# Kernel tuning notes

Hardware: AMD Instinct MI355X
Metric: run time of the kernel (lower is better)

The kernel has to match this reference:

```python
import jax, jax.numpy as jnp
import numpy as np

N_NODES = 50000
N_EDGES = 1600000
IN_DIM = 128
HID = 128
OUT_DIM = 64
N_REL = 8


def _rgcn(x, src, dst, et, W, W0, num_nodes):
    # W: [R, in, out], per-relation transform; identical math to the torch
    # loop over unique relations (scatter-adds commute).
    xW = jnp.einsum('ni,rio->rno', x, W)          # [R, N, out]
    msgs = xW[et, src]                             # [E, out] gather per edge
    out = x @ W0 + jax.ops.segment_sum(msgs, dst, num_segments=num_nodes)
    deg = jax.ops.segment_sum(jnp.ones_like(dst, dtype=x.dtype), dst,
                              num_segments=num_nodes)
    deg = jnp.maximum(deg, 1.0)
    return out / deg[:, None]


def _group(x, src, dst, num_nodes, alpha, Wp, bp):
    agg = jax.ops.segment_sum(x[src], dst, num_segments=num_nodes)
    deg = jax.ops.segment_sum(jnp.ones_like(dst, dtype=x.dtype), dst,
                              num_segments=num_nodes)
    deg = jnp.maximum(deg, 1.0)
    agg = agg / deg[:, None]
    return x + alpha * (agg @ Wp + bp)


def setup_inputs() -> dict:
    key = jax.random.key(0)
    ks = jax.random.split(key, 16)
    x = jax.random.normal(ks[0], (N_NODES, IN_DIM), dtype=jnp.float32)
    edge_index = jax.random.randint(ks[1], (2, N_EDGES), 0, N_NODES)
    edge_type = jax.random.randint(ks[2], (N_EDGES,), 0, N_REL)
    s = 0.02
    return {
        'x': x,
        'edge_index': edge_index,
        'edge_type': edge_type,
        'W1': jax.random.normal(ks[3], (N_REL, IN_DIM, HID)) * s,
        'W01': jax.random.normal(ks[4], (IN_DIM, HID)) * s,
        'alpha1': jnp.float32(0.5),
        'proj1_w': jax.random.normal(ks[5], (HID, HID)) * s,
        'proj1_b': jnp.zeros((HID,), jnp.float32),
        'W2': jax.random.normal(ks[6], (N_REL, HID, HID)) * s,
        'W02': jax.random.normal(ks[7], (HID, HID)) * s,
        'alpha2': jnp.float32(0.5),
        'proj2_w': jax.random.normal(ks[8], (HID, HID)) * s,
        'proj2_b': jnp.zeros((HID,), jnp.float32),
        'out_w': jax.random.normal(ks[9], (HID, OUT_DIM)) * s,
        'out_b': jnp.zeros((OUT_DIM,), jnp.float32),
    }


def reference(x, edge_index, edge_type, W1, W01, alpha1, proj1_w, proj1_b,
              W2, W02, alpha2, proj2_w, proj2_b, out_w, out_b):
    n = x.shape[0]
    src, dst = edge_index[0], edge_index[1]
    h = _rgcn(x, src, dst, edge_type, W1, W01, n)
    h = jax.nn.relu(h)
    h = _group(h, src, dst, n, alpha1, proj1_w, proj1_b)
    h = _rgcn(h, src, dst, edge_type, W2, W02, n)
    h = jax.nn.relu(h)
    h = _group(h, src, dst, n, alpha2, proj2_w, proj2_b)
    return h @ out_w + out_b
```

## Files before the change

### kernel.cpp

```cpp
#include <hip/hip_runtime.h>
#include <hip/hip_bf16.h>

#define NN 50000
#define NE 1600000
#define NR 8
#define D 128
#define DOUT 64
#define NCB ((NN + 63) / 64)
#define NBLK 256
#define CH ((NE + NBLK - 1) / NBLK)
#define GRIDM ((NN + 63) / 64)

typedef __attribute__((ext_vector_type(8))) __bf16 bf16x8;
typedef __attribute__((ext_vector_type(4))) float f32x4;

__device__ __forceinline__ float bflo(unsigned u) { return __uint_as_float(u << 16); }
__device__ __forceinline__ float bfhi(unsigned u) { return __uint_as_float(u & 0xffff0000u); }
__device__ __forceinline__ unsigned f2bf_rne(float x) {
    unsigned u = __float_as_uint(x);
    return (u + 0x7fffu + ((u >> 16) & 1u)) >> 16;
}
__device__ __forceinline__ unsigned pack2(float a, float b) {
    return f2bf_rne(a) | (f2bf_rne(b) << 16);
}

__device__ __forceinline__ void gl2lds16(const void* g, void* l) {
    __builtin_amdgcn_global_load_lds(
        (const __attribute__((address_space(1))) unsigned int*)g,
        (__attribute__((address_space(3))) unsigned int*)l, 16, 0, 0);
}

__global__ __launch_bounds__(1024)
void k_cnt(const int* __restrict__ ei, int* __restrict__ cntmat) {
    __shared__ int h[NCB];
    const int blk = blockIdx.x, tid = threadIdx.x;
    for (int i = tid; i < NCB; i += 1024) h[i] = 0;
    __syncthreads();
    const int e0 = blk * CH, e1 = min(e0 + CH, NE);
    for (int e = e0 + tid; e < e1; e += 1024)
        atomicAdd(&h[ei[NE + e] >> 6], 1);
    __syncthreads();
    for (int i = tid; i < NCB; i += 1024) cntmat[i * NBLK + blk] = h[i];
}

__global__ __launch_bounds__(64)
void k_colscan(int* __restrict__ cntmat, int* __restrict__ colsum) {
    const int b = blockIdx.x, lane = threadIdx.x;
    int4 v = *reinterpret_cast<int4*>(cntmat + b * NBLK + lane * 4);
    int s = v.x + v.y + v.z + v.w;
    int e = s;
    #pragma unroll
    for (int o = 1; o < 64; o <<= 1) {
        int y = __shfl_up(e, o);
        if (lane >= o) e += y;
    }
    int excl = e - s;
    int4 w;
    w.x = excl; w.y = excl + v.x; w.z = excl + v.x + v.y; w.w = excl + v.x + v.y + v.z;
    *reinterpret_cast<int4*>(cntmat + b * NBLK + lane * 4) = w;
    if (lane == 63) colsum[b] = e;
}

__global__ __launch_bounds__(1024)
void k_bscan(const int* __restrict__ colsum, int* __restrict__ bstart,
             int* __restrict__ off) {
    __shared__ int s[1024];
    int t = threadIdx.x;
    int v = (t < NCB) ? colsum[t] : 0;
    s[t] = v;
    __syncthreads();
    for (int o = 1; o < 1024; o <<= 1) {
        int x = (t >= o) ? s[t - o] : 0;
        __syncthreads();
        s[t] += x;
        __syncthreads();
    }
    if (t < NCB) bstart[t] = s[t] - v;
    if (t == 0) { bstart[NCB] = NE; off[NN] = NE; }
}

__global__ __launch_bounds__(1024)
void k_pscatter(const int* __restrict__ ei, const int* __restrict__ et,
                const int* __restrict__ cntmat, const int* __restrict__ bstart,
                int* __restrict__ bck) {
    __shared__ int cur[NCB];
    const int blk = blockIdx.x, tid = threadIdx.x;
    for (int i = tid; i < NCB; i += 1024)
        cur[i] = bstart[i] + cntmat[i * NBLK + blk];
    __syncthreads();
    const int e0 = blk * CH, e1 = min(e0 + CH, NE);
    for (int e = e0 + tid; e < e1; e += 1024) {
        int dst = ei[NE + e];
        int pk = ((dst & 63) << 19) | (et[e] << 16) | ei[e];
        int p = atomicAdd(&cur[dst >> 6], 1);
        bck[p] = pk;
    }
}

__global__ __launch_bounds__(256)
void k_build(const int* __restrict__ bck, const int* __restrict__ cbase,
             int* __restrict__ off, float* __restrict__ invdeg,
             int* __restrict__ esrcF) {
    __shared__ int cnt[64];
    __shared__ int cur[64];
    __shared__ int sb[2];
    const int b = blockIdx.x;
    const int tid = threadIdx.x;
    if (tid < 64) cnt[tid] = 0;
    if (tid == 0) { sb[0] = cbase[b]; sb[1] = cbase[b + 1]; }
    __syncthreads();
    const int s0 = sb[0], s1 = sb[1];
    for (int i = s0 + tid; i < s1; i += 256)
        atomicAdd(&cnt[(bck[i] >> 19) & 63], 1);
    __syncthreads();
    if (tid < 64) {
        int c = cnt[tid];
        int x = c;
        #pragma unroll
        for (int o = 1; o < 64; o <<= 1) {
            int y = __shfl_up(x, o);
            if (tid >= o) x += y;
        }
        int excl = x - c;
        int gd = b * 64 + tid;
        if (gd < NN) {
            off[gd] = s0 + excl;
            invdeg[gd] = 1.0f / (float)max(c, 1);
        }
        cur[tid] = s0 + excl;
    }
    __syncthreads();
    for (int i = s0 + tid; i < s1; i += 256) {
        int pk = bck[i];
        int p = atomicAdd(&cur[(pk >> 19) & 63], 1);
        esrcF[p] = pk & 0x7FFFF;
    }
}


__global__ void k_prep_x(const float* __restrict__ X, unsigned* __restrict__ Xt) {
    int i = blockIdx.x * blockDim.x + threadIdx.x;
    if (i < NN * 64) {
        float2 f = reinterpret_cast<const float2*>(X)[i];
        Xt[i] = pack2(f.x, f.y);
    }
}

__global__ void k_prep_wcat(const float* __restrict__ W0, const float* __restrict__ Wr,
                            unsigned short* __restrict__ dst) {
    int i = blockIdx.x * blockDim.x + threadIdx.x;
    if (i < 128 * 1152) {
        int n = i / 1152, k = i % 1152;
        float v = (k < 128) ? W0[k * 128 + n] : Wr[(k - 128) * 128 + n];
        int kc = k >> 7, kl = k & 127;
        int e = kl ^ ((n & 7) << 3);
        dst[((size_t)kc * 128 + n) * 128 + e] = (unsigned short)f2bf_rne(v);
    }
}

__global__ void k_prep_wt(const float* __restrict__ src, unsigned short* __restrict__ dst,
                          int N) {
    int i = blockIdx.x * blockDim.x + threadIdx.x;
    if (i < N * 128) {
        int n = i >> 7, k = i & 127;
        int e = k ^ ((n & 7) << 3);
        dst[n * 128 + e] = (unsigned short)f2bf_rne(src[k * N + n]);
    }
}


#define LOAD8                                                            \
    int p0 = __builtin_amdgcn_readfirstlane(esrcF[j]);                   \
    int p1 = __builtin_amdgcn_readfirstlane(esrcF[j + 1]);               \
    int p2 = __builtin_amdgcn_readfirstlane(esrcF[j + 2]);               \
    int p3 = __builtin_amdgcn_readfirstlane(esrcF[j + 3]);               \
    int p4 = __builtin_amdgcn_readfirstlane(esrcF[j + 4]);               \
    int p5 = __builtin_amdgcn_readfirstlane(esrcF[j + 5]);               \
    int p6 = __builtin_amdgcn_readfirstlane(esrcF[j + 6]);               \
    int p7 = __builtin_amdgcn_readfirstlane(esrcF[j + 7]);               \
    unsigned u0 = Xt[(unsigned)(p0 & 0xffff) * 64 + lane];               \
    unsigned u1 = Xt[(unsigned)(p1 & 0xffff) * 64 + lane];               \
    unsigned u2 = Xt[(unsigned)(p2 & 0xffff) * 64 + lane];               \
    unsigned u3 = Xt[(unsigned)(p3 & 0xffff) * 64 + lane];               \
    unsigned u4 = Xt[(unsigned)(p4 & 0xffff) * 64 + lane];               \
    unsigned u5 = Xt[(unsigned)(p5 & 0xffff) * 64 + lane];               \
    unsigned u6 = Xt[(unsigned)(p6 & 0xffff) * 64 + lane];               \
    unsigned u7 = Xt[(unsigned)(p7 & 0xffff) * 64 + lane];

__global__ __launch_bounds__(256)
void k_aggw(const unsigned* __restrict__ Xt, unsigned* __restrict__ AW,
            const int* __restrict__ off, const int* __restrict__ esrcF) {
    const int wid = threadIdx.x >> 6, lane = threadIdx.x & 63;
    const int v = blockIdx.x * 4 + wid;
    if (v >= NN) return;
    const int s = off[v], e = off[v + 1];
    float l0 = 0, l1 = 0, l2 = 0, l3 = 0, l4 = 0, l5 = 0, l6 = 0, l7 = 0;
    float h0 = 0, h1 = 0, h2 = 0, h3 = 0, h4 = 0, h5 = 0, h6 = 0, h7 = 0;
#define ACCW(P, U)                                                       \
    do {                                                                 \
        float _lo = bflo(U), _hi = bfhi(U);                              \
        switch ((P) >> 16) {                                             \
            case 0: l0 += _lo; h0 += _hi; break;                         \
            case 1: l1 += _lo; h1 += _hi; break;                         \
            case 2: l2 += _lo; h2 += _hi; break;                         \
            case 3: l3 += _lo; h3 += _hi; break;                         \
            case 4: l4 += _lo; h4 += _hi; break;                         \
            case 5: l5 += _lo; h5 += _hi; break;                         \
            case 6: l6 += _lo; h6 += _hi; break;                         \
            default: l7 += _lo; h7 += _hi; break;                        \
        }                                                                \
    } while (0)
    for (int j = s; j < e; j += 8) {
        LOAD8
        ACCW(p0, u0);
        if (j + 1 < e) ACCW(p1, u1);
        if (j + 2 < e) ACCW(p2, u2);
        if (j + 3 < e) ACCW(p3, u3);
        if (j + 4 < e) ACCW(p4, u4);
        if (j + 5 < e) ACCW(p5, u5);
        if (j + 6 < e) ACCW(p6, u6);
        if (j + 7 < e) ACCW(p7, u7);
    }
#undef ACCW
    unsigned* o = AW + (size_t)v * 512 + lane;
    o[0]   = pack2(l0, h0);
    o[64]  = pack2(l1, h1);
    o[128] = pack2(l2, h2);
    o[192] = pack2(l3, h3);
    o[256] = pack2(l4, h4);
    o[320] = pack2(l5, h5);
    o[384] = pack2(l6, h6);
    o[448] = pack2(l7, h7);
}

__global__ __launch_bounds__(256)
void k_aggh(const unsigned* __restrict__ Xt, unsigned* __restrict__ AH,
            const int* __restrict__ off, const int* __restrict__ esrcF,
            const float* __restrict__ invdeg) {
    const int wid = threadIdx.x >> 6, lane = threadIdx.x & 63;
    const int v = blockIdx.x * 4 + wid;
    if (v >= NN) return;
    const int s = off[v], e = off[v + 1];
    float a0 = 0.f, a1 = 0.f;
    for (int j = s; j < e; j += 8) {
        LOAD8
        (void)p0;
        a0 += bflo(u0); a1 += bfhi(u0);
        if (j + 1 < e) { a0 += bflo(u1); a1 += bfhi(u1); }
        if (j + 2 < e) { a0 += bflo(u2); a1 += bfhi(u2); }
        if (j + 3 < e) { a0 += bflo(u3); a1 += bfhi(u3); }
        if (j + 4 < e) { a0 += bflo(u4); a1 += bfhi(u4); }
        if (j + 5 < e) { a0 += bflo(u5); a1 += bfhi(u5); }
        if (j + 6 < e) { a0 += bflo(u6); a1 += bfhi(u6); }
        if (j + 7 < e) { a0 += bflo(u7); a1 += bfhi(u7); }
    }
    float inv = invdeg[v];
    AH[(size_t)v * 64 + lane] = pack2(a0 * inv, a1 * inv);
}

template <int N, int MODE, int NCHUNK>
__global__ __launch_bounds__(256)
void k_mfma(const short* __restrict__ A0, const short* __restrict__ A1,
            const short* __restrict__ Wc,
            float* __restrict__ Yf, unsigned short* __restrict__ Ybf,
            const float* __restrict__ aux, const float* __restrict__ bias,
            const float* __restrict__ alpha_p, const float* __restrict__ invdeg) {
    constexpr int NT = N / 16;
    constexpr int NIT = N / 16;
    __shared__ short Bs[N * 128];
    const int tid = threadIdx.x;
    const int wave = tid >> 6;
    const int lane = tid & 63;
    const int lr = lane & 15;
    const int lk = (lane >> 4) * 8;
    const int rowBase = blockIdx.x * 64 + wave * 16;
    const int r0 = min(rowBase + lr, NN - 1);

    f32x4 acc[NT];
    #pragma unroll
    for (int nt = 0; nt < NT; ++nt) acc[nt] = f32x4{0.f, 0.f, 0.f, 0.f};

    for (int kc = 0; kc < NCHUNK; ++kc) {
        {
            const char* gs = (const char*)Wc + (size_t)kc * N * 256
                             + (wave * NIT) * 1024 + lane * 16;
            char* ls = (char*)Bs + (wave * NIT) * 1024;
            #pragma unroll
            for (int j = 0; j < NIT; ++j)
                gl2lds16(gs + j * 1024, ls + j * 1024);
        }
        const short* abase = (kc == 0) ? (A0 + (size_t)r0 * 128)
                                       : (A1 + (size_t)r0 * 1024 + (kc - 1) * 128);
        bf16x8 a0 = *reinterpret_cast<const bf16x8*>(abase + 0 + lk);
        bf16x8 a1 = *reinterpret_cast<const bf16x8*>(abase + 32 + lk);
        bf16x8 a2 = *reinterpret_cast<const bf16x8*>(abase + 64 + lk);
        bf16x8 a3 = *reinterpret_cast<const bf16x8*>(abase + 96 + lk);
        __syncthreads();

        #pragma unroll
        for (int s = 0; s < 4; ++s) {
            bf16x8 a = (s == 0) ? a0 : (s == 1) ? a1 : (s == 2) ? a2 : a3;
            #pragma unroll
            for (int nt = 0; nt < NT; ++nt) {
                const int c = nt * 16 + lr;
                const int e0 = (s * 32 + lk) ^ ((c & 7) << 3);
                bf16x8 b = *reinterpret_cast<const bf16x8*>(
                    (const char*)Bs + c * 256 + e0 * 2);
                acc[nt] = __builtin_amdgcn_mfma_f32_16x16x32_bf16(a, b, acc[nt], 0, 0, 0);
            }
        }
        __syncthreads();
    }

    const float al = (MODE == 1) ? *alpha_p : 0.f;
    #pragma unroll
    for (int j = 0; j < 4; ++j) {
        const int row = rowBase + (lane >> 4) * 4 + j;
        if (row >= NN) continue;
        float idg = (MODE == 0) ? invdeg[row] : 0.f;
        #pragma unroll
        for (int nt = 0; nt < NT; ++nt) {
            const int col = nt * 16 + lr;
            float v = acc[nt][j];
            if (MODE == 0) {
                v = fmaxf(v * idg, 0.f);
                Yf[(size_t)row * 128 + col] = v;
                Ybf[(size_t)row * 128 + col] = (unsigned short)f2bf_rne(v);
            } else if (MODE == 1) {
                v = aux[(size_t)row * 128 + col] + al * (v + bias[col]);
                Ybf[(size_t)row * 128 + col] = (unsigned short)f2bf_rne(v);
            } else {
                Yf[(size_t)row * 64 + col] = v + bias[col];
            }
        }
    }
}


extern "C" void kernel_launch(void* const* d_in, const int* in_sizes, int n_in,
                              void* d_out, int out_size, void* d_ws, size_t ws_size,
                              hipStream_t stream) {
    const float* X   = (const float*)d_in[0];
    const int*   ei  = (const int*)d_in[1];
    const int*   et  = (const int*)d_in[2];
    const float* W1  = (const float*)d_in[3];
    const float* W01 = (const float*)d_in[4];
    const float* al1 = (const float*)d_in[5];
    const float* p1w = (const float*)d_in[6];
    const float* p1b = (const float*)d_in[7];
    const float* W2  = (const float*)d_in[8];
    const float* W02 = (const float*)d_in[9];
    const float* al2 = (const float*)d_in[10];
    const float* p2w = (const float*)d_in[11];
    const float* p2b = (const float*)d_in[12];
    const float* ow  = (const float*)d_in[13];
    const float* ob  = (const float*)d_in[14];
    float* out = (float*)d_out;

    char* wsp = (char*)d_ws;
    size_t o = 0;
    auto take = [&](size_t bytes) -> void* {
        void* p = wsp + o;
        o = (o + bytes + 255) & ~(size_t)255;
        return p;
    };
    int*      cntmat = (int*)take((size_t)NCB * NBLK * 4);
    int*      colsum = (int*)take((size_t)NCB * 4);
    int*      bstart = (int*)take((size_t)(NCB + 1) * 4);
    int*      off    = (int*)take((size_t)(NN + 1) * 4);
    float*    invdeg = (float*)take((size_t)NN * 4);
    int*      bck    = (int*)take((size_t)NE * 4);
    int*      esrcF  = (int*)take((size_t)(NE + 8) * 4);
    unsigned* T1     = (unsigned*)take((size_t)NN * 64 * 4);
    unsigned* T2     = (unsigned*)take((size_t)NN * 64 * 4);
    unsigned* T3     = (unsigned*)take((size_t)NN * 64 * 4);
    unsigned* AW     = (unsigned*)take((size_t)NN * 512 * 4);
    unsigned* AH     = (unsigned*)take((size_t)NN * 64 * 4);
    float*    Hf     = (float*)take((size_t)NN * 128 * 4);
    unsigned short* WtC1 = (unsigned short*)take((size_t)128 * 1152 * 2);
    unsigned short* WtC2 = (unsigned short*)take((size_t)128 * 1152 * 2);
    unsigned short* Wtp1 = (unsigned short*)take((size_t)128 * 128 * 2);
    unsigned short* Wtp2 = (unsigned short*)take((size_t)128 * 128 * 2);
    unsigned short* WtO  = (unsigned short*)take((size_t)64 * 128 * 2);
    if (o > ws_size) return;

    k_cnt<<<NBLK, 1024, 0, stream>>>(ei, cntmat);
    k_colscan<<<NCB, 64, 0, stream>>>(cntmat, colsum);
    k_bscan<<<1, 1024, 0, stream>>>(colsum, bstart, off);
    k_pscatter<<<NBLK, 1024, 0, stream>>>(ei, et, cntmat, bstart, bck);
    k_build<<<NCB, 256, 0, stream>>>(bck, bstart, off, invdeg, esrcF);

    k_prep_x<<<(NN * 64 + 255) / 256, 256, 0, stream>>>(X, T1);
    k_prep_wcat<<<(128 * 1152 + 255) / 256, 256, 0, stream>>>(W01, W1, WtC1);
    k_prep_wcat<<<(128 * 1152 + 255) / 256, 256, 0, stream>>>(W02, W2, WtC2);
    k_prep_wt<<<(128 * 128 + 255) / 256, 256, 0, stream>>>(p1w, Wtp1, 128);
    k_prep_wt<<<(128 * 128 + 255) / 256, 256, 0, stream>>>(p2w, Wtp2, 128);
    k_prep_wt<<<(64 * 128 + 255) / 256, 256, 0, stream>>>(ow, WtO, 64);

    const int GAGG = (NN + 3) / 4;

    k_aggw<<<GAGG, 256, 0, stream>>>(T1, AW, off, esrcF);
    k_mfma<128, 0, 9><<<GRIDM, 256, 0, stream>>>(
        (const short*)T1, (const short*)AW, (const short*)WtC1,
        Hf, (unsigned short*)T2, nullptr, nullptr, nullptr, invdeg);
    k_aggh<<<GAGG, 256, 0, stream>>>(T2, AH, off, esrcF, invdeg);
    k_mfma<128, 1, 1><<<GRIDM, 256, 0, stream>>>(
        (const short*)AH, nullptr, (const short*)Wtp1,
        nullptr, (unsigned short*)T3, Hf, p1b, al1, nullptr);

    k_aggw<<<GAGG, 256, 0, stream>>>(T3, AW, off, esrcF);
    k_mfma<128, 0, 9><<<GRIDM, 256, 0, stream>>>(
        (const short*)T3, (const short*)AW, (const short*)WtC2,
        Hf, (unsigned short*)T1, nullptr, nullptr, nullptr, invdeg);
    k_aggh<<<GAGG, 256, 0, stream>>>(T1, AH, off, esrcF, invdeg);
    k_mfma<128, 1, 1><<<GRIDM, 256, 0, stream>>>(
        (const short*)AH, nullptr, (const short*)Wtp2,
        nullptr, (unsigned short*)T2, Hf, p2b, al2, nullptr);

    k_mfma<64, 2, 1><<<GRIDM, 256, 0, stream>>>(
        (const short*)T2, nullptr, (const short*)WtO,
        out, nullptr, nullptr, ob, nullptr, nullptr);
}
```

Before: 562.3 us.

## Sort CSR edges by destination and relation; aggregate per-relation segments

The build step now buckets edges by (destination, relation), giving eight offsets per node (off8). The relation-wise aggregation kernel can then walk one contiguous segment per relation with a single pair of accumulators, instead of dispatching every edge through an eight-way switch. This drops the per-edge scalar branching and the need to carry relation bits in the edge array. In exchange each relation segment is short (a few edges on average), so the 4-wide unrolled loads get less memory-level parallelism and more tail waste per node.

```diff
diff --git a/kernel.cpp b/kernel.cpp
--- a/kernel.cpp
+++ b/kernel.cpp
@@ -62,8 +62,7 @@
 }
 
 __global__ __launch_bounds__(1024)
-void k_bscan(const int* __restrict__ colsum, int* __restrict__ bstart,
-             int* __restrict__ off) {
+void k_bscan(const int* __restrict__ colsum, int* __restrict__ bstart) {
     __shared__ int s[1024];
     int t = threadIdx.x;
     int v = (t < NCB) ? colsum[t] : 0;
@@ -76,7 +75,7 @@
         __syncthreads();
     }
     if (t < NCB) bstart[t] = s[t] - v;
-    if (t == 0) { bstart[NCB] = NE; off[NN] = NE; }
+    if (t == 0) bstart[NCB] = NE;
 }
 
 __global__ __launch_bounds__(1024)
@@ -99,41 +98,54 @@
 
 __global__ __launch_bounds__(256)
 void k_build(const int* __restrict__ bck, const int* __restrict__ cbase,
-             int* __restrict__ off, float* __restrict__ invdeg,
+             int* __restrict__ off8, float* __restrict__ invdeg,
              int* __restrict__ esrcF) {
-    __shared__ int cnt[64];
-    __shared__ int cur[64];
+    __shared__ int cnt[512];
+    __shared__ int cur[512];
+    __shared__ int wtot[4];
     __shared__ int sb[2];
     const int b = blockIdx.x;
     const int tid = threadIdx.x;
-    if (tid < 64) cnt[tid] = 0;
+    const int wid = tid >> 6, lane = tid & 63;
+    cnt[tid] = 0; cnt[tid + 256] = 0;
     if (tid == 0) { sb[0] = cbase[b]; sb[1] = cbase[b + 1]; }
     __syncthreads();
     const int s0 = sb[0], s1 = sb[1];
     for (int i = s0 + tid; i < s1; i += 256)
-        atomicAdd(&cnt[(bck[i] >> 19) & 63], 1);
-    __syncthreads();
+        atomicAdd(&cnt[(bck[i] >> 16) & 511], 1);
+    __syncthreads();
+    int c0 = cnt[2 * tid], c1 = cnt[2 * tid + 1];
+    int ps = c0 + c1;
+    int x = ps;
+    #pragma unroll
+    for (int o = 1; o < 64; o <<= 1) {
+        int y = __shfl_up(x, o);
+        if (lane >= o) x += y;
+    }
+    if (lane == 63) wtot[wid] = x;
+    __syncthreads();
+    int woff = 0;
+    #pragma unroll
+    for (int w2 = 0; w2 < 4; ++w2) woff += (w2 < wid) ? wtot[w2] : 0;
+    int base = s0 + woff + x - ps;
+    cur[2 * tid] = base;
+    cur[2 * tid + 1] = base + c0;
+    off8[(size_t)b * 512 + 2 * tid] = base;
+    off8[(size_t)b * 512 + 2 * tid + 1] = base + c0;
     if (tid < 64) {
-        int c = cnt[tid];
-        int x = c;
-        #pragma unroll
-        for (int o = 1; o < 64; o <<= 1) {
-            int y = __shfl_up(x, o);
-            if (tid >= o) x += y;
-        }
-        int excl = x - c;
         int gd = b * 64 + tid;
         if (gd < NN) {
-            off[gd] = s0 + excl;
-            invdeg[gd] = 1.0f / (float)max(c, 1);
+            int dsum = 0;
+            #pragma unroll
+            for (int r = 0; r < 8; ++r) dsum += cnt[tid * 8 + r];
+            invdeg[gd] = 1.0f / (float)max(dsum, 1);
         }
-        cur[tid] = s0 + excl;
     }
     __syncthreads();
     for (int i = s0 + tid; i < s1; i += 256) {
         int pk = bck[i];
-        int p = atomicAdd(&cur[(pk >> 19) & 63], 1);
-        esrcF[p] = pk & 0x7FFFF;
+        int p = atomicAdd(&cur[(pk >> 16) & 511], 1);
+        esrcF[p] = pk & 0xFFFF;
     }
 }
 
@@ -169,82 +181,62 @@
 }
 
 
-#define LOAD8                                                            \
-    int p0 = __builtin_amdgcn_readfirstlane(esrcF[j]);                   \
-    int p1 = __builtin_amdgcn_readfirstlane(esrcF[j + 1]);               \
-    int p2 = __builtin_amdgcn_readfirstlane(esrcF[j + 2]);               \
-    int p3 = __builtin_amdgcn_readfirstlane(esrcF[j + 3]);               \
-    int p4 = __builtin_amdgcn_readfirstlane(esrcF[j + 4]);               \
-    int p5 = __builtin_amdgcn_readfirstlane(esrcF[j + 5]);               \
-    int p6 = __builtin_amdgcn_readfirstlane(esrcF[j + 6]);               \
-    int p7 = __builtin_amdgcn_readfirstlane(esrcF[j + 7]);               \
-    unsigned u0 = Xt[(unsigned)(p0 & 0xffff) * 64 + lane];               \
-    unsigned u1 = Xt[(unsigned)(p1 & 0xffff) * 64 + lane];               \
-    unsigned u2 = Xt[(unsigned)(p2 & 0xffff) * 64 + lane];               \
-    unsigned u3 = Xt[(unsigned)(p3 & 0xffff) * 64 + lane];               \
-    unsigned u4 = Xt[(unsigned)(p4 & 0xffff) * 64 + lane];               \
-    unsigned u5 = Xt[(unsigned)(p5 & 0xffff) * 64 + lane];               \
-    unsigned u6 = Xt[(unsigned)(p6 & 0xffff) * 64 + lane];               \
-    unsigned u7 = Xt[(unsigned)(p7 & 0xffff) * 64 + lane];
-
 __global__ __launch_bounds__(256)
 void k_aggw(const unsigned* __restrict__ Xt, unsigned* __restrict__ AW,
-            const int* __restrict__ off, const int* __restrict__ esrcF) {
+            const int* __restrict__ off8, const int* __restrict__ esrcF) {
     const int wid = threadIdx.x >> 6, lane = threadIdx.x & 63;
     const int v = blockIdx.x * 4 + wid;
     if (v >= NN) return;
-    const int s = off[v], e = off[v + 1];
-    float l0 = 0, l1 = 0, l2 = 0, l3 = 0, l4 = 0, l5 = 0, l6 = 0, l7 = 0;
-    float h0 = 0, h1 = 0, h2 = 0, h3 = 0, h4 = 0, h5 = 0, h6 = 0, h7 = 0;
-#define ACCW(P, U)                                                       \
-    do {                                                                 \
-        float _lo = bflo(U), _hi = bfhi(U);                              \
-        switch ((P) >> 16) {                                             \
-            case 0: l0 += _lo; h0 += _hi; break;                         \
-            case 1: l1 += _lo; h1 += _hi; break;                         \
-            case 2: l2 += _lo; h2 += _hi; break;                         \
-            case 3: l3 += _lo; h3 += _hi; break;                         \
-            case 4: l4 += _lo; h4 += _hi; break;                         \
-            case 5: l5 += _lo; h5 += _hi; break;                         \
-            case 6: l6 += _lo; h6 += _hi; break;                         \
-            default: l7 += _lo; h7 += _hi; break;                        \
-        }                                                                \
-    } while (0)
-    for (int j = s; j < e; j += 8) {
-        LOAD8
-        ACCW(p0, u0);
-        if (j + 1 < e) ACCW(p1, u1);
-        if (j + 2 < e) ACCW(p2, u2);
-        if (j + 3 < e) ACCW(p3, u3);
-        if (j + 4 < e) ACCW(p4, u4);
-        if (j + 5 < e) ACCW(p5, u5);
-        if (j + 6 < e) ACCW(p6, u6);
-        if (j + 7 < e) ACCW(p7, u7);
-    }
-#undef ACCW
     unsigned* o = AW + (size_t)v * 512 + lane;
-    o[0]   = pack2(l0, h0);
-    o[64]  = pack2(l1, h1);
-    o[128] = pack2(l2, h2);
-    o[192] = pack2(l3, h3);
-    o[256] = pack2(l4, h4);
-    o[320] = pack2(l5, h5);
-    o[384] = pack2(l6, h6);
-    o[448] = pack2(l7, h7);
+    int s = off8[v * 8];
+    for (int r = 0; r < 8; ++r) {
+        const int e = off8[v * 8 + r + 1];
+        float a0 = 0.f, a1 = 0.f;
+        for (int j = s; j < e; j += 4) {
+            int p0 = __builtin_amdgcn_readfirstlane(esrcF[j]);
+            int p1 = __builtin_amdgcn_readfirstlane(esrcF[j + 1]);
+            int p2 = __builtin_amdgcn_readfirstlane(esrcF[j + 2]);
+            int p3 = __builtin_amdgcn_readfirstlane(esrcF[j + 3]);
+            unsigned u0 = Xt[(unsigned)(p0 & 0xffff) * 64 + lane];
+            unsigned u1 = Xt[(unsigned)(p1 & 0xffff) * 64 + lane];
+            unsigned u2 = Xt[(unsigned)(p2 & 0xffff) * 64 + lane];
+            unsigned u3 = Xt[(unsigned)(p3 & 0xffff) * 64 + lane];
+            a0 += bflo(u0); a1 += bfhi(u0);
+            if (j + 1 < e) { a0 += bflo(u1); a1 += bfhi(u1); }
+            if (j + 2 < e) { a0 += bflo(u2); a1 += bfhi(u2); }
+            if (j + 3 < e) { a0 += bflo(u3); a1 += bfhi(u3); }
+        }
+        o[r * 64] = pack2(a0, a1);
+        s = e;
+    }
 }
 
 __global__ __launch_bounds__(256)
 void k_aggh(const unsigned* __restrict__ Xt, unsigned* __restrict__ AH,
-            const int* __restrict__ off, const int* __restrict__ esrcF,
+            const int* __restrict__ off8, const int* __restrict__ esrcF,
             const float* __restrict__ invdeg) {
     const int wid = threadIdx.x >> 6, lane = threadIdx.x & 63;
     const int v = blockIdx.x * 4 + wid;
     if (v >= NN) return;
-    const int s = off[v], e = off[v + 1];
+    const int s = off8[v * 8], e = off8[v * 8 + 8];
     float a0 = 0.f, a1 = 0.f;
     for (int j = s; j < e; j += 8) {
-        LOAD8
-        (void)p0;
+        int p0 = __builtin_amdgcn_readfirstlane(esrcF[j]);
+        int p1 = __builtin_amdgcn_readfirstlane(esrcF[j + 1]);
+        int p2 = __builtin_amdgcn_readfirstlane(esrcF[j + 2]);
+        int p3 = __builtin_amdgcn_readfirstlane(esrcF[j + 3]);
+        int p4 = __builtin_amdgcn_readfirstlane(esrcF[j + 4]);
+        int p5 = __builtin_amdgcn_readfirstlane(esrcF[j + 5]);
+        int p6 = __builtin_amdgcn_readfirstlane(esrcF[j + 6]);
+        int p7 = __builtin_amdgcn_readfirstlane(esrcF[j + 7]);
+        unsigned u0 = Xt[(unsigned)(p0 & 0xffff) * 64 + lane];
+        unsigned u1 = Xt[(unsigned)(p1 & 0xffff) * 64 + lane];
+        unsigned u2 = Xt[(unsigned)(p2 & 0xffff) * 64 + lane];
+        unsigned u3 = Xt[(unsigned)(p3 & 0xffff) * 64 + lane];
+        unsigned u4 = Xt[(unsigned)(p4 & 0xffff) * 64 + lane];
+        unsigned u5 = Xt[(unsigned)(p5 & 0xffff) * 64 + lane];
+        unsigned u6 = Xt[(unsigned)(p6 & 0xffff) * 64 + lane];
+        unsigned u7 = Xt[(unsigned)(p7 & 0xffff) * 64 + lane];
         a0 += bflo(u0); a1 += bfhi(u0);
         if (j + 1 < e) { a0 += bflo(u1); a1 += bfhi(u1); }
         if (j + 2 < e) { a0 += bflo(u2); a1 += bfhi(u2); }
@@ -367,7 +359,7 @@
     int*      cntmat = (int*)take((size_t)NCB * NBLK * 4);
     int*      colsum = (int*)take((size_t)NCB * 4);
     int*      bstart = (int*)take((size_t)(NCB + 1) * 4);
-    int*      off    = (int*)take((size_t)(NN + 1) * 4);
+    int*      off8   = (int*)take((size_t)(NCB * 512 + 1) * 4);
     float*    invdeg = (float*)take((size_t)NN * 4);
     int*      bck    = (int*)take((size_t)NE * 4);
     int*      esrcF  = (int*)take((size_t)(NE + 8) * 4);
@@ -386,9 +378,9 @@
 
     k_cnt<<<NBLK, 1024, 0, stream>>>(ei, cntmat);
     k_colscan<<<NCB, 64, 0, stream>>>(cntmat, colsum);
-    k_bscan<<<1, 1024, 0, stream>>>(colsum, bstart, off);
+    k_bscan<<<1, 1024, 0, stream>>>(colsum, bstart);
     k_pscatter<<<NBLK, 1024, 0, stream>>>(ei, et, cntmat, bstart, bck);
-    k_build<<<NCB, 256, 0, stream>>>(bck, bstart, off, invdeg, esrcF);
+    k_build<<<NCB, 256, 0, stream>>>(bck, bstart, off8, invdeg, esrcF);
 
     k_prep_x<<<(NN * 64 + 255) / 256, 256, 0, stream>>>(X, T1);
     k_prep_wcat<<<(128 * 1152 + 255) / 256, 256, 0, stream>>>(W01, W1, WtC1);
@@ -399,20 +391,20 @@
 
     const int GAGG = (NN + 3) / 4;
 
-    k_aggw<<<GAGG, 256, 0, stream>>>(T1, AW, off, esrcF);
+    k_aggw<<<GAGG, 256, 0, stream>>>(T1, AW, off8, esrcF);
     k_mfma<128, 0, 9><<<GRIDM, 256, 0, stream>>>(
         (const short*)T1, (const short*)AW, (const short*)WtC1,
         Hf, (unsigned short*)T2, nullptr, nullptr, nullptr, invdeg);
-    k_aggh<<<GAGG, 256, 0, stream>>>(T2, AH, off, esrcF, invdeg);
+    k_aggh<<<GAGG, 256, 0, stream>>>(T2, AH, off8, esrcF, invdeg);
     k_mfma<128, 1, 1><<<GRIDM, 256, 0, stream>>>(
         (const short*)AH, nullptr, (const short*)Wtp1,
         nullptr, (unsigned short*)T3, Hf, p1b, al1, nullptr);
 
-    k_aggw<<<GAGG, 256, 0, stream>>>(T3, AW, off, esrcF);
+    k_aggw<<<GAGG, 256, 0, stream>>>(T3, AW, off8, esrcF);
     k_mfma<128, 0, 9><<<GRIDM, 256, 0, stream>>>(
         (const short*)T3, (const short*)AW, (const short*)WtC2,
         Hf, (unsigned short*)T1, nullptr, nullptr, nullptr, invdeg);
-    k_aggh<<<GAGG, 256, 0, stream>>>(T1, AH, off, esrcF, invdeg);
+    k_aggh<<<GAGG, 256, 0, stream>>>(T1, AH, off8, esrcF, invdeg);
     k_mfma<128, 1, 1><<<GRIDM, 256, 0, stream>>>(
         (const short*)AH, nullptr, (const short*)Wtp2,
         nullptr, (unsigned short*)T2, Hf, p2b, al2, nullptr);
```

After: 555.5 us. About the same (-1.2%).
